# Kernel optimization log

Measured on AMD Instinct MI355X. Metric: run time of the kernel, lower is better.

Reference implementation:

```python
import jax, jax.numpy as jnp
import numpy as np

N, E, B = 50000, 800000, 64      # nodes, edges, graphs per branch
F_IN, C = 128, 128               # input feats, convolution_neurons
H = 2                            # hidden_layers
EPS = 1e-3                       # keras BatchNormalization epsilon


def _gconv(x, src, dst, W, b, gamma, beta):
    # Spektral GeneralConv: linear -> gather(src) -> scatter-sum(dst) -> BN(inference, mean=0,var=1) -> relu
    h = x @ W + b                                            # [N, C]
    agg = jax.ops.segment_sum(h[src], dst, num_segments=x.shape[0])  # [N, C]
    agg = agg * (gamma / np.float32(np.sqrt(1.0 + EPS))) + beta
    return jax.nn.relu(agg)


def _avg_pool(x, seg):
    s = jax.ops.segment_sum(x, seg, num_segments=B)          # [B, C]
    cnt = jax.ops.segment_sum(jnp.ones((x.shape[0],), x.dtype), seg, num_segments=B)
    return s / jnp.maximum(cnt, 1.0)[:, None]


def setup_inputs() -> dict:
    key = jax.random.key(0)
    ks = jax.random.split(key, 12)

    def glorot(k, shp):
        lim = float(np.sqrt(6.0 / (shp[0] + shp[1])))
        return jax.random.uniform(k, shp, jnp.float32, -lim, lim)

    inp = {}
    inp["x1"] = jax.random.normal(ks[0], (N, F_IN), jnp.float32)
    inp["x2"] = jax.random.normal(ks[1], (N, F_IN), jnp.float32)
    inp["edges1"] = jax.random.randint(ks[2], (2, E), 0, N)
    inp["edges2"] = jax.random.randint(ks[3], (2, E), 0, N)
    inp["seg1"] = jnp.sort(jax.random.randint(ks[4], (N,), 0, B))
    inp["seg2"] = jnp.sort(jax.random.randint(ks[5], (N,), 0, B))
    # branch 1: GeneralConv(128) then GeneralConv(64)
    inp["W1a"], inp["b1a"] = glorot(ks[6], (F_IN, C)), jnp.zeros((C,), jnp.float32)
    inp["g1a"], inp["be1a"] = jnp.ones((C,), jnp.float32), jnp.zeros((C,), jnp.float32)
    inp["W1b"], inp["b1b"] = glorot(ks[7], (C, C // 2)), jnp.zeros((C // 2,), jnp.float32)
    inp["g1b"], inp["be1b"] = jnp.ones((C // 2,), jnp.float32), jnp.zeros((C // 2,), jnp.float32)
    # branch 2
    inp["W2a"], inp["b2a"] = glorot(ks[8], (F_IN, C)), jnp.zeros((C,), jnp.float32)
    inp["g2a"], inp["be2a"] = jnp.ones((C,), jnp.float32), jnp.zeros((C,), jnp.float32)
    inp["W2b"], inp["b2b"] = glorot(ks[9], (C, C // 2)), jnp.zeros((C // 2,), jnp.float32)
    inp["g2b"], inp["be2b"] = jnp.ones((C // 2,), jnp.float32), jnp.zeros((C // 2,), jnp.float32)
    # shared hidden dense + output head
    inp["Wd"], inp["bd"] = glorot(ks[10], (C, C)), jnp.zeros((C,), jnp.float32)
    inp["Wo"], inp["bo"] = glorot(ks[11], (C, 1)), jnp.zeros((1,), jnp.float32)
    return inp


def reference(x1, x2, edges1, edges2, seg1, seg2,
              W1a, b1a, g1a, be1a, W1b, b1b, g1b, be1b,
              W2a, b2a, g2a, be2a, W2b, b2b, g2b, be2b,
              Wd, bd, Wo, bo):
    h1 = _gconv(x1, edges1[0], edges1[1], W1a, b1a, g1a, be1a)   # [N, 128]
    h1 = _gconv(h1, edges1[0], edges1[1], W1b, b1b, g1b, be1b)   # [N, 64]
    p1 = _avg_pool(h1, seg1)                                      # [B, 64]
    h2 = _gconv(x2, edges2[0], edges2[1], W2a, b2a, g2a, be2a)
    h2 = _gconv(h2, edges2[0], edges2[1], W2b, b2b, g2b, be2b)
    p2 = _avg_pool(h2, seg2)
    out = jnp.concatenate([p1, p2], axis=-1)                      # [B, 128]
    for _ in range(H):  # shared Dense(128, relu) applied hidden_layers times
        out = jax.nn.relu(out @ Wd + bd)
    return jax.nn.sigmoid(out @ Wo + bo)                          # [B, 1]
```

## Files before the change

kernel.cpp:

```cpp
#include <hip/hip_runtime.h>
#include <math.h>

#define GS    512
#define GSH   9
#define NGMAX 128
#define FCAP  48
#define SCAP  10240


__global__ __launch_bounds__(1024) void bin_kernel(
    const int* __restrict__ s1, const int* __restrict__ d1,
    const int* __restrict__ s2, const int* __restrict__ d2,
    int* __restrict__ gcur, int* __restrict__ pairs, int E, int G1) {
  __shared__ int fifo[NGMAX][FCAP];
  __shared__ int fcnt[NGMAX];
  __shared__ int fbase[NGMAX];
  __shared__ int fpre[NGMAX + 1];
  const int* src = blockIdx.y ? s2 : s1;
  const int* dst = blockIdx.y ? d2 : d1;
  int gboff = blockIdx.y * G1;
  int tid = threadIdx.x;
  if (tid < NGMAX) fcnt[tid] = 0;
  __syncthreads();
  int e0 = blockIdx.x * 4096;
  for (int r = 0; r < 4; ++r) {
    int e = e0 + r * 1024 + tid;
    if (e < E) {
      int s = src[e], d = dst[e];
      int g = d >> GSH;
      int pk = s | ((d & (GS - 1)) << 17);
      int pos = atomicAdd(&fcnt[g], 1);
      if (pos < FCAP) fifo[g][pos] = pk;
      else {
        int gp = atomicAdd(&gcur[gboff + g], 1);
        pairs[(size_t)(gboff + g) * SCAP + gp] = pk;
      }
    }
    __syncthreads();
    if (tid < G1) {
      int c = fcnt[tid];
      if (c > FCAP) c = FCAP;
      fcnt[tid] = c;
      fbase[tid] = (c > 0) ? atomicAdd(&gcur[gboff + tid], c) : 0;
    }
    __syncthreads();
    if (tid == 0) {
      int acc = 0;
      for (int i = 0; i < G1; ++i) { fpre[i] = acc; acc += fcnt[i]; }
      fpre[G1] = acc;
    }
    __syncthreads();
    int T = fpre[G1];
    for (int t = tid; t < T; t += 1024) {
      int lo = 0, hi = G1;
      while (hi - lo > 1) { int mid = (lo + hi) >> 1; if (fpre[mid] <= t) lo = mid; else hi = mid; }
      int idx = t - fpre[lo];
      pairs[(size_t)(gboff + lo) * SCAP + fbase[lo] + idx] = fifo[lo][idx];
    }
    __syncthreads();
    if (tid < NGMAX) fcnt[tid] = 0;
    __syncthreads();
  }
}


__global__ __launch_bounds__(1024) void refine_kernel(
    const int* __restrict__ gcur, int* __restrict__ pairs,
    int* __restrict__ offs, int* __restrict__ counts, int N, int G1) {
  __shared__ int stg[SCAP];
  __shared__ int hist[GS];
  __shared__ int excl[GS];
  __shared__ int wtot[8];
  int gl = blockIdx.x, br = blockIdx.y;
  int g = br * G1 + gl;
  size_t rbase = (size_t)g * SCAP;
  int rcnt = gcur[g];
  if (rcnt > SCAP) rcnt = SCAP;
  int tid = threadIdx.x;
  if (tid < GS) hist[tid] = 0;
  __syncthreads();
  for (int i = tid; i < rcnt; i += 1024) {
    int pk = pairs[rbase + i];
    stg[i] = pk;
    atomicAdd(&hist[pk >> 17], 1);
  }
  __syncthreads();
  if (tid < GS) {
    int lane = tid & 63, wv = tid >> 6;
    int v = hist[tid];
    int inc = v;
    #pragma unroll
    for (int off = 1; off < 64; off <<= 1) {
      int t = __shfl_up(inc, off);
      if (lane >= off) inc += t;
    }
    excl[tid] = inc - v;
    if (lane == 63) wtot[wv] = inc;
  }
  __syncthreads();
  if (tid == 0) {
    int a = 0;
    #pragma unroll
    for (int w = 0; w < 8; ++w) { int t = wtot[w]; wtot[w] = a; a += t; }
  }
  __syncthreads();
  if (tid < GS) excl[tid] += wtot[tid >> 6];
  __syncthreads();
  int node0 = gl * GS;
  int nloc = N - node0; if (nloc > GS) nloc = GS;
  for (int j = tid; j < nloc; j += 1024) {
    offs[br * N + node0 + j] = (int)rbase + excl[j];
    counts[br * N + node0 + j] = hist[j];
  }
  __syncthreads();
  for (int i = tid; i < rcnt; i += 1024) {
    int pk = stg[i];
    int pos = atomicAdd(&excl[pk >> 17], 1);
    pairs[rbase + pos] = pk & 0x1FFFF;
  }
}


template <int COUT>
__global__ __launch_bounds__(256, 2) void gemm2_kernel(
    const float* __restrict__ X0, const float* __restrict__ X1,
    const float* __restrict__ W0, const float* __restrict__ W1,
    const float* __restrict__ bias0, const float* __restrict__ bias1,
    float* __restrict__ Y0, float* __restrict__ Y1, int nrows) {
  constexpr int CG = COUT / 4;
  constexpr int RG = 256 / CG;
  constexpr int BM = 64;
  constexpr int RPT = BM / RG;
  const float* X = blockIdx.y ? X1 : X0;
  const float* W = blockIdx.y ? W1 : W0;
  const float* bias = blockIdx.y ? bias1 : bias0;
  float* Y = blockIdx.y ? Y1 : Y0;
  __shared__ float xs[BM][132];
  int tid = threadIdx.x;
  int block_row = blockIdx.x * BM;
  for (int i = tid; i < BM * 32; i += 256) {
    int r = i >> 5, c4 = i & 31;
    int gr = block_row + r;
    float4 v = make_float4(0.f, 0.f, 0.f, 0.f);
    if (gr < nrows) v = reinterpret_cast<const float4*>(X + (size_t)gr * 128)[c4];
    *reinterpret_cast<float4*>(&xs[r][c4 * 4]) = v;
  }
  __syncthreads();
  int c0 = (tid % CG) * 4;
  int r0 = (tid / CG) * RPT;
  float acc[RPT][4] = {};
  #pragma unroll 2
  for (int k = 0; k < 128; k += 4) {
    float4 w0 = *reinterpret_cast<const float4*>(&W[(k + 0) * COUT + c0]);
    float4 w1 = *reinterpret_cast<const float4*>(&W[(k + 1) * COUT + c0]);
    float4 w2 = *reinterpret_cast<const float4*>(&W[(k + 2) * COUT + c0]);
    float4 w3 = *reinterpret_cast<const float4*>(&W[(k + 3) * COUT + c0]);
    #pragma unroll
    for (int i = 0; i < RPT; ++i) {
      float4 x = *reinterpret_cast<const float4*>(&xs[r0 + i][k]);
      acc[i][0] = fmaf(x.x, w0.x, acc[i][0]);
      acc[i][1] = fmaf(x.x, w0.y, acc[i][1]);
      acc[i][2] = fmaf(x.x, w0.z, acc[i][2]);
      acc[i][3] = fmaf(x.x, w0.w, acc[i][3]);
      acc[i][0] = fmaf(x.y, w1.x, acc[i][0]);
      acc[i][1] = fmaf(x.y, w1.y, acc[i][1]);
      acc[i][2] = fmaf(x.y, w1.z, acc[i][2]);
      acc[i][3] = fmaf(x.y, w1.w, acc[i][3]);
      acc[i][0] = fmaf(x.z, w2.x, acc[i][0]);
      acc[i][1] = fmaf(x.z, w2.y, acc[i][1]);
      acc[i][2] = fmaf(x.z, w2.z, acc[i][2]);
      acc[i][3] = fmaf(x.z, w2.w, acc[i][3]);
      acc[i][0] = fmaf(x.w, w3.x, acc[i][0]);
      acc[i][1] = fmaf(x.w, w3.y, acc[i][1]);
      acc[i][2] = fmaf(x.w, w3.z, acc[i][2]);
      acc[i][3] = fmaf(x.w, w3.w, acc[i][3]);
    }
  }
  float4 bv = *reinterpret_cast<const float4*>(&bias[c0]);
  #pragma unroll
  for (int i = 0; i < RPT; ++i) {
    int gr = block_row + r0 + i;
    if (gr < nrows) {
      float4 o;
      o.x = acc[i][0] + bv.x; o.y = acc[i][1] + bv.y;
      o.z = acc[i][2] + bv.z; o.w = acc[i][3] + bv.w;
      *reinterpret_cast<float4*>(&Y[(size_t)gr * COUT + c0]) = o;
    }
  }
}


__global__ __launch_bounds__(256) void agg128_kernel(
    const float* __restrict__ h, const int* __restrict__ offs,
    const int* __restrict__ counts, const int* __restrict__ csr_src,
    const float* __restrict__ gamma, const float* __restrict__ beta,
    float* __restrict__ out, int n) {
  int node = blockIdx.x * 4 + (threadIdx.x >> 6);
  if (node >= n) return;
  node = __builtin_amdgcn_readfirstlane(node);
  int ch = blockIdx.y;
  int lane = threadIdx.x & 63;
  int half = lane >> 5;
  int l5 = lane & 31;
  const float* hh = h + ch * 64;
  int beg = offs[node], cnt = counts[node];
  const int* lp = csr_src + beg;
  float a0 = 0.f, a1 = 0.f;
  for (int base = 0; base < cnt; base += 64) {
    int rem = cnt - base;
    int m = rem < 64 ? rem : 64;
    int idx = lp[base + (lane < m ? lane : m - 1)];
    int mfull = m & ~15;
    int j = 0;
    for (; j < mfull; j += 16) {
      float2 v[8];
      #pragma unroll
      for (int u = 0; u < 8; ++u) {
        int s = __shfl(idx, j + 2 * u + half);
        v[u] = *reinterpret_cast<const float2*>(hh + (size_t)s * 128 + l5 * 2);
      }
      #pragma unroll
      for (int u = 0; u < 8; ++u) { a0 += v[u].x; a1 += v[u].y; }
    }
    if (j < m) {
      float2 v[8];
      #pragma unroll
      for (int u = 0; u < 8; ++u) {
        int ed = j + 2 * u + half;
        int s = __shfl(idx, ed < m ? ed : m - 1);
        v[u] = *reinterpret_cast<const float2*>(hh + (size_t)s * 128 + l5 * 2);
      }
      #pragma unroll
      for (int u = 0; u < 8; ++u) {
        bool ok = (j + 2 * u + half) < m;
        a0 += ok ? v[u].x : 0.f;
        a1 += ok ? v[u].y : 0.f;
      }
    }
  }
  a0 += __shfl_xor(a0, 32);
  a1 += __shfl_xor(a1, 32);
  const float inv = 1.0f / sqrtf(1.0f + 1.0e-3f);
  if (half == 0) {
    float2 g = reinterpret_cast<const float2*>(gamma + ch * 64)[l5];
    float2 b = reinterpret_cast<const float2*>(beta + ch * 64)[l5];
    float2 o;
    o.x = fmaxf(fmaf(a0, g.x * inv, b.x), 0.f);
    o.y = fmaxf(fmaf(a1, g.y * inv, b.y), 0.f);
    *reinterpret_cast<float2*>(out + (size_t)node * 128 + ch * 64 + l5 * 2) = o;
  }
}


__global__ __launch_bounds__(256) void agg64_kernel(
    const float* __restrict__ h, const int* __restrict__ offs,
    const int* __restrict__ counts, const int* __restrict__ csr_src,
    const float* __restrict__ gamma, const float* __restrict__ beta,
    float* __restrict__ out, int n) {
  int node = blockIdx.x * 4 + (threadIdx.x >> 6);
  if (node >= n) return;
  node = __builtin_amdgcn_readfirstlane(node);
  int lane = threadIdx.x & 63;
  int half = lane >> 5;
  int l5 = lane & 31;
  int beg = offs[node], cnt = counts[node];
  const int* lp = csr_src + beg;
  float a0 = 0.f, a1 = 0.f;
  for (int base = 0; base < cnt; base += 64) {
    int rem = cnt - base;
    int m = rem < 64 ? rem : 64;
    int idx = lp[base + (lane < m ? lane : m - 1)];
    int mfull = m & ~15;
    int j = 0;
    for (; j < mfull; j += 16) {
      float2 v[8];
      #pragma unroll
      for (int u = 0; u < 8; ++u) {
        int s = __shfl(idx, j + 2 * u + half);
        v[u] = *reinterpret_cast<const float2*>(h + (size_t)s * 64 + l5 * 2);
      }
      #pragma unroll
      for (int u = 0; u < 8; ++u) { a0 += v[u].x; a1 += v[u].y; }
    }
    if (j < m) {
      float2 v[8];
      #pragma unroll
      for (int u = 0; u < 8; ++u) {
        int ed = j + 2 * u + half;
        int s = __shfl(idx, ed < m ? ed : m - 1);
        v[u] = *reinterpret_cast<const float2*>(h + (size_t)s * 64 + l5 * 2);
      }
      #pragma unroll
      for (int u = 0; u < 8; ++u) {
        bool ok = (j + 2 * u + half) < m;
        a0 += ok ? v[u].x : 0.f;
        a1 += ok ? v[u].y : 0.f;
      }
    }
  }
  a0 += __shfl_xor(a0, 32);
  a1 += __shfl_xor(a1, 32);
  const float inv = 1.0f / sqrtf(1.0f + 1.0e-3f);
  if (half == 0) {
    float2 g = reinterpret_cast<const float2*>(gamma)[l5];
    float2 b = reinterpret_cast<const float2*>(beta)[l5];
    float2 o;
    o.x = fmaxf(fmaf(a0, g.x * inv, b.x), 0.f);
    o.y = fmaxf(fmaf(a1, g.y * inv, b.y), 0.f);
    *reinterpret_cast<float2*>(out + (size_t)node * 64 + l5 * 2) = o;
  }
}


__global__ __launch_bounds__(1024) void pool2_kernel(
    const float* __restrict__ h0, const float* __restrict__ h1,
    const int* __restrict__ seg0, const int* __restrict__ seg1,
    float* __restrict__ p, int n) {
  const float* h = blockIdx.y ? h1 : h0;
  const int* seg = blockIdx.y ? seg1 : seg0;
  float* pb = p + blockIdx.y * 64 * 64;
  int g = blockIdx.x;
  int lo, hi;
  { int l = 0, r = n; while (l < r) { int m = (l + r) >> 1; if (seg[m] < g) l = m + 1; else r = m; } lo = l; }
  { int l = 0, r = n; while (l < r) { int m = (l + r) >> 1; if (seg[m] < g + 1) l = m + 1; else r = m; } hi = l; }
  int c = threadIdx.x & 63;
  int sub = threadIdx.x >> 6;
  float acc = 0.f;
  for (int i = lo + sub; i < hi; i += 16) acc += h[(size_t)i * 64 + c];
  __shared__ float red[16][64];
  red[sub][c] = acc;
  __syncthreads();
  if (sub == 0) {
    float s = 0.f;
    #pragma unroll
    for (int k = 0; k < 16; ++k) s += red[k][c];
    float cnt = (float)(hi - lo);
    pb[g * 64 + c] = s / fmaxf(cnt, 1.0f);
  }
}


__global__ __launch_bounds__(512) void head_kernel(const float* __restrict__ p,
                                                   const float* __restrict__ Wd,
                                                   const float* __restrict__ bd,
                                                   const float* __restrict__ Wo,
                                                   const float* __restrict__ bo,
                                                   float* __restrict__ out) {
  __shared__ float cur[64][128];
  __shared__ float nxt[64][128];
  int tid = threadIdx.x;
  const float* p1 = p;
  const float* p2 = p + 64 * 64;
  for (int i = tid; i < 64 * 128; i += 512) {
    int r = i >> 7, c = i & 127;
    cur[r][c] = (c < 64) ? p1[r * 64 + c] : p2[r * 64 + (c - 64)];
  }
  __syncthreads();
  int c0 = (tid & 31) * 4;
  int r0 = (tid >> 5) * 4;
  for (int layer = 0; layer < 2; ++layer) {
    float acc[4][4] = {};
    #pragma unroll 4
    for (int k = 0; k < 128; ++k) {
      float4 w = *reinterpret_cast<const float4*>(&Wd[k * 128 + c0]);
      #pragma unroll
      for (int i = 0; i < 4; ++i) {
        float x = cur[r0 + i][k];
        acc[i][0] = fmaf(x, w.x, acc[i][0]);
        acc[i][1] = fmaf(x, w.y, acc[i][1]);
        acc[i][2] = fmaf(x, w.z, acc[i][2]);
        acc[i][3] = fmaf(x, w.w, acc[i][3]);
      }
    }
    float4 bv = *reinterpret_cast<const float4*>(&bd[c0]);
    __syncthreads();
    #pragma unroll
    for (int i = 0; i < 4; ++i) {
      float4 o;
      o.x = fmaxf(acc[i][0] + bv.x, 0.f);
      o.y = fmaxf(acc[i][1] + bv.y, 0.f);
      o.z = fmaxf(acc[i][2] + bv.z, 0.f);
      o.w = fmaxf(acc[i][3] + bv.w, 0.f);
      *reinterpret_cast<float4*>(&nxt[r0 + i][c0]) = o;
    }
    __syncthreads();
    for (int i = tid; i < 64 * 128; i += 512) (&cur[0][0])[i] = (&nxt[0][0])[i];
    __syncthreads();
  }
  int wv = tid >> 6, lane = tid & 63;
  for (int r = wv; r < 64; r += 8) {
    float v = cur[r][lane] * Wo[lane] + cur[r][64 + lane] * Wo[64 + lane];
    #pragma unroll
    for (int off = 32; off; off >>= 1) v += __shfl_down(v, off);
    if (lane == 0) out[r] = 1.0f / (1.0f + expf(-(v + bo[0])));
  }
}


extern "C" void kernel_launch(void* const* d_in, const int* in_sizes, int n_in,
                              void* d_out, int out_size, void* d_ws, size_t ws_size,
                              hipStream_t stream) {
  const float* x1  = (const float*)d_in[0];
  const float* x2  = (const float*)d_in[1];
  const int* e1    = (const int*)d_in[2];
  const int* e2    = (const int*)d_in[3];
  const int* seg1  = (const int*)d_in[4];
  const int* seg2  = (const int*)d_in[5];
  const float* W1a = (const float*)d_in[6];  const float* b1a = (const float*)d_in[7];
  const float* g1a = (const float*)d_in[8];  const float* be1a = (const float*)d_in[9];
  const float* W1b = (const float*)d_in[10]; const float* b1b = (const float*)d_in[11];
  const float* g1b = (const float*)d_in[12]; const float* be1b = (const float*)d_in[13];
  const float* W2a = (const float*)d_in[14]; const float* b2a = (const float*)d_in[15];
  const float* g2a = (const float*)d_in[16]; const float* be2a = (const float*)d_in[17];
  const float* W2b = (const float*)d_in[18]; const float* b2b = (const float*)d_in[19];
  const float* g2b = (const float*)d_in[20]; const float* be2b = (const float*)d_in[21];
  const float* Wd  = (const float*)d_in[22]; const float* bd  = (const float*)d_in[23];
  const float* Wo  = (const float*)d_in[24]; const float* bo  = (const float*)d_in[25];
  float* out = (float*)d_out;

  const int N = in_sizes[0] / 128;
  const int E = in_sizes[2] / 2;
  const int G1 = (N + GS - 1) >> GSH;
  const int G  = 2 * G1;

  char* ws = (char*)d_ws;
  size_t off = 0;
  auto alloc = [&](size_t bytes) -> void* {
    void* ptr = ws + off;
    off += (bytes + 255) & ~(size_t)255;
    return ptr;
  };
  float* h0   = (float*)alloc((size_t)N * 128 * sizeof(float));
  float* h1   = (float*)alloc((size_t)N * 128 * sizeof(float));
  float* ag0  = (float*)alloc((size_t)N * 128 * sizeof(float));
  float* ag1  = (float*)alloc((size_t)N * 128 * sizeof(float));
  int* pairs  = (int*)alloc((size_t)G * SCAP * sizeof(int));
  int* offs   = (int*)alloc((size_t)(2 * N) * sizeof(int));
  int* counts = (int*)alloc((size_t)(2 * N) * sizeof(int));
  int* gcur   = (int*)alloc((size_t)(G + 8) * sizeof(int));
  float* pbuf = (float*)alloc(2 * 64 * 64 * sizeof(float));
  (void)ws_size; (void)n_in; (void)out_size;

  hipMemsetAsync(gcur, 0, (size_t)(G + 8) * sizeof(int), stream);
  {
    dim3 gb((E + 4095) / 4096, 2);
    bin_kernel<<<gb, 1024, 0, stream>>>(e1, e1 + E, e2, e2 + E, gcur, pairs, E, G1);
    dim3 gr(G1, 2);
    refine_kernel<<<gr, 1024, 0, stream>>>(gcur, pairs, offs, counts, N, G1);
  }

  const int* offs0 = offs;       const int* cnts0 = counts;
  const int* offs1 = offs + N;   const int* cnts1 = counts + N;

  {
    dim3 gg((N + 63) / 64, 2);
    gemm2_kernel<128><<<gg, 256, 0, stream>>>(x1, x2, W1a, W2a, b1a, b2a, h0, h1, N);
  }
  {
    dim3 ga((N + 3) / 4, 2);
    agg128_kernel<<<ga, 256, 0, stream>>>(h0, offs0, cnts0, pairs, g1a, be1a, ag0, N);
    agg128_kernel<<<ga, 256, 0, stream>>>(h1, offs1, cnts1, pairs, g2a, be2a, ag1, N);
  }
  {
    dim3 gg((N + 63) / 64, 2);
    gemm2_kernel<64><<<gg, 256, 0, stream>>>(ag0, ag1, W1b, W2b, b1b, b2b, h0, h1, N);
  }
  agg64_kernel<<<(N + 3) / 4, 256, 0, stream>>>(h0, offs0, cnts0, pairs, g1b, be1b, ag0, N);
  agg64_kernel<<<(N + 3) / 4, 256, 0, stream>>>(h1, offs1, cnts1, pairs, g2b, be2b, ag1, N);
  {
    dim3 gp(64, 2);
    pool2_kernel<<<gp, 1024, 0, stream>>>(ag0, ag1, seg1, seg2, pbuf, N);
  }
  head_kernel<<<1, 512, 0, stream>>>(pbuf, Wd, bd, Wo, bo, out);
}
```

Before: 336.6 us.

## Slice aggregation by 16-column chunks with 16 nodes per wavefront

```diff
diff --git a/kernel.cpp b/kernel.cpp
--- a/kernel.cpp
+++ b/kernel.cpp
@@ -135,7 +135,7 @@
   const float* W = blockIdx.y ? W1 : W0;
   const float* bias = blockIdx.y ? bias1 : bias0;
   float* Y = blockIdx.y ? Y1 : Y0;
-  __shared__ float xs[BM][132];
+  __shared__ float xs[BM][128];
   int tid = threadIdx.x;
   int block_row = blockIdx.x * BM;
   for (int i = tid; i < BM * 32; i += 256) {
@@ -190,124 +190,56 @@
 }
 
 
-__global__ __launch_bounds__(256) void agg128_kernel(
+template <int C, int NSL>
+__global__ __launch_bounds__(1024) void agg_sl_kernel(
     const float* __restrict__ h, const int* __restrict__ offs,
-    const int* __restrict__ counts, const int* __restrict__ csr_src,
+    const int* __restrict__ counts, const int* __restrict__ csr,
     const float* __restrict__ gamma, const float* __restrict__ beta,
     float* __restrict__ out, int n) {
-  int node = blockIdx.x * 4 + (threadIdx.x >> 6);
-  if (node >= n) return;
-  node = __builtin_amdgcn_readfirstlane(node);
-  int ch = blockIdx.y;
-  int lane = threadIdx.x & 63;
-  int half = lane >> 5;
-  int l5 = lane & 31;
-  const float* hh = h + ch * 64;
-  int beg = offs[node], cnt = counts[node];
-  const int* lp = csr_src + beg;
-  float a0 = 0.f, a1 = 0.f;
-  for (int base = 0; base < cnt; base += 64) {
-    int rem = cnt - base;
-    int m = rem < 64 ? rem : 64;
-    int idx = lp[base + (lane < m ? lane : m - 1)];
-    int mfull = m & ~15;
-    int j = 0;
-    for (; j < mfull; j += 16) {
-      float2 v[8];
-      #pragma unroll
-      for (int u = 0; u < 8; ++u) {
-        int s = __shfl(idx, j + 2 * u + half);
-        v[u] = *reinterpret_cast<const float2*>(hh + (size_t)s * 128 + l5 * 2);
-      }
-      #pragma unroll
-      for (int u = 0; u < 8; ++u) { a0 += v[u].x; a1 += v[u].y; }
-    }
-    if (j < m) {
-      float2 v[8];
-      #pragma unroll
-      for (int u = 0; u < 8; ++u) {
-        int ed = j + 2 * u + half;
-        int s = __shfl(idx, ed < m ? ed : m - 1);
-        v[u] = *reinterpret_cast<const float2*>(hh + (size_t)s * 128 + l5 * 2);
-      }
-      #pragma unroll
-      for (int u = 0; u < 8; ++u) {
-        bool ok = (j + 2 * u + half) < m;
-        a0 += ok ? v[u].x : 0.f;
-        a1 += ok ? v[u].y : 0.f;
-      }
-    }
-  }
-  a0 += __shfl_xor(a0, 32);
-  a1 += __shfl_xor(a1, 32);
-  const float inv = 1.0f / sqrtf(1.0f + 1.0e-3f);
-  if (half == 0) {
-    float2 g = reinterpret_cast<const float2*>(gamma + ch * 64)[l5];
-    float2 b = reinterpret_cast<const float2*>(beta + ch * 64)[l5];
-    float2 o;
-    o.x = fmaxf(fmaf(a0, g.x * inv, b.x), 0.f);
-    o.y = fmaxf(fmaf(a1, g.y * inv, b.y), 0.f);
-    *reinterpret_cast<float2*>(out + (size_t)node * 128 + ch * 64 + l5 * 2) = o;
-  }
-}
-
-
-__global__ __launch_bounds__(256) void agg64_kernel(
-    const float* __restrict__ h, const int* __restrict__ offs,
-    const int* __restrict__ counts, const int* __restrict__ csr_src,
-    const float* __restrict__ gamma, const float* __restrict__ beta,
-    float* __restrict__ out, int n) {
-  int node = blockIdx.x * 4 + (threadIdx.x >> 6);
-  if (node >= n) return;
-  node = __builtin_amdgcn_readfirstlane(node);
-  int lane = threadIdx.x & 63;
-  int half = lane >> 5;
-  int l5 = lane & 31;
-  int beg = offs[node], cnt = counts[node];
-  const int* lp = csr_src + beg;
-  float a0 = 0.f, a1 = 0.f;
-  for (int base = 0; base < cnt; base += 64) {
-    int rem = cnt - base;
-    int m = rem < 64 ? rem : 64;
-    int idx = lp[base + (lane < m ? lane : m - 1)];
-    int mfull = m & ~15;
-    int j = 0;
-    for (; j < mfull; j += 16) {
-      float2 v[8];
-      #pragma unroll
-      for (int u = 0; u < 8; ++u) {
-        int s = __shfl(idx, j + 2 * u + half);
-        v[u] = *reinterpret_cast<const float2*>(h + (size_t)s * 64 + l5 * 2);
-      }
-      #pragma unroll
-      for (int u = 0; u < 8; ++u) { a0 += v[u].x; a1 += v[u].y; }
-    }
-    if (j < m) {
-      float2 v[8];
-      #pragma unroll
-      for (int u = 0; u < 8; ++u) {
-        int ed = j + 2 * u + half;
-        int s = __shfl(idx, ed < m ? ed : m - 1);
-        v[u] = *reinterpret_cast<const float2*>(h + (size_t)s * 64 + l5 * 2);
-      }
-      #pragma unroll
-      for (int u = 0; u < 8; ++u) {
-        bool ok = (j + 2 * u + half) < m;
-        a0 += ok ? v[u].x : 0.f;
-        a1 += ok ? v[u].y : 0.f;
-      }
-    }
-  }
-  a0 += __shfl_xor(a0, 32);
-  a1 += __shfl_xor(a1, 32);
-  const float inv = 1.0f / sqrtf(1.0f + 1.0e-3f);
-  if (half == 0) {
-    float2 g = reinterpret_cast<const float2*>(gamma)[l5];
-    float2 b = reinterpret_cast<const float2*>(beta)[l5];
-    float2 o;
-    o.x = fmaxf(fmaf(a0, g.x * inv, b.x), 0.f);
-    o.y = fmaxf(fmaf(a1, g.y * inv, b.y), 0.f);
-    *reinterpret_cast<float2*>(out + (size_t)node * 64 + l5 * 2) = o;
+  int slice = blockIdx.x & (NSL - 1);
+  int nodeblk = blockIdx.x / NSL;
+  int tid = threadIdx.x;
+  int wv = tid >> 6, lane = tid & 63;
+  int grp = lane >> 2, c4 = lane & 3;
+  int node = nodeblk * 256 + wv * 16 + grp;
+  bool live = node < n;
+  int nd = live ? node : n - 1;
+  int beg = offs[nd];
+  int cnt = live ? counts[nd] : 0;
+  int elast = cnt > 0 ? cnt - 1 : 0;
+  int mx = cnt;
+  #pragma unroll
+  for (int off = 4; off < 64; off <<= 1) {
+    int t = __shfl_xor(mx, off);
+    mx = t > mx ? t : mx;
+  }
+  const float* hp = h + slice * 16 + c4 * 4;
+  float4 a = make_float4(0.f, 0.f, 0.f, 0.f);
+  for (int eb = 0; eb < mx; eb += 4) {
+    int ee = eb + c4;
+    ee = ee < elast ? ee : elast;
+    int idx = csr[beg + ee];
+    #pragma unroll
+    for (int u = 0; u < 4; ++u) {
+      int s = __shfl(idx, grp * 4 + u);
+      float4 v = *reinterpret_cast<const float4*>(hp + (size_t)s * C);
+      bool ok = (eb + u) < cnt;
+      a.x += ok ? v.x : 0.f;
+      a.y += ok ? v.y : 0.f;
+      a.z += ok ? v.z : 0.f;
+      a.w += ok ? v.w : 0.f;
+    }
+  }
+  if (live) {
+    const float inv = 1.0f / sqrtf(1.0f + 1.0e-3f);
+    float4 gv = *reinterpret_cast<const float4*>(gamma + slice * 16 + c4 * 4);
+    float4 bv = *reinterpret_cast<const float4*>(beta + slice * 16 + c4 * 4);
+    float4 o;
+    o.x = fmaxf(fmaf(a.x, gv.x * inv, bv.x), 0.f);
+    o.y = fmaxf(fmaf(a.y, gv.y * inv, bv.y), 0.f);
+    o.z = fmaxf(fmaf(a.z, gv.z * inv, bv.z), 0.f);
+    o.w = fmaxf(fmaf(a.w, gv.w * inv, bv.w), 0.f);
+    *reinterpret_cast<float4*>(out + (size_t)node * C + slice * 16 + c4 * 4) = o;
   }
 }
 
@@ -422,6 +354,7 @@
   const int E = in_sizes[2] / 2;
   const int G1 = (N + GS - 1) >> GSH;
   const int G  = 2 * G1;
+  const int NB = (N + 255) / 256;
 
   char* ws = (char*)d_ws;
   size_t off = 0;
@@ -449,24 +382,18 @@
     refine_kernel<<<gr, 1024, 0, stream>>>(gcur, pairs, offs, counts, N, G1);
   }
 
-  const int* offs0 = offs;       const int* cnts0 = counts;
-  const int* offs1 = offs + N;   const int* cnts1 = counts + N;
-
   {
     dim3 gg((N + 63) / 64, 2);
     gemm2_kernel<128><<<gg, 256, 0, stream>>>(x1, x2, W1a, W2a, b1a, b2a, h0, h1, N);
   }
-  {
-    dim3 ga((N + 3) / 4, 2);
-    agg128_kernel<<<ga, 256, 0, stream>>>(h0, offs0, cnts0, pairs, g1a, be1a, ag0, N);
-    agg128_kernel<<<ga, 256, 0, stream>>>(h1, offs1, cnts1, pairs, g2a, be2a, ag1, N);
-  }
+  agg_sl_kernel<128, 8><<<NB * 8, 1024, 0, stream>>>(h0, offs, counts, pairs, g1a, be1a, ag0, N);
+  agg_sl_kernel<128, 8><<<NB * 8, 1024, 0, stream>>>(h1, offs + N, counts + N, pairs, g2a, be2a, ag1, N);
   {
     dim3 gg((N + 63) / 64, 2);
     gemm2_kernel<64><<<gg, 256, 0, stream>>>(ag0, ag1, W1b, W2b, b1b, b2b, h0, h1, N);
   }
-  agg64_kernel<<<(N + 3) / 4, 256, 0, stream>>>(h0, offs0, cnts0, pairs, g1b, be1b, ag0, N);
-  agg64_kernel<<<(N + 3) / 4, 256, 0, stream>>>(h1, offs1, cnts1, pairs, g2b, be2b, ag1, N);
+  agg_sl_kernel<64, 4><<<NB * 4, 1024, 0, stream>>>(h0, offs, counts, pairs, g1b, be1b, ag0, N);
+  agg_sl_kernel<64, 4><<<NB * 4, 1024, 0, stream>>>(h1, offs + N, counts + N, pairs, g2b, be2b, ag1, N);
   {
     dim3 gp(64, 2);
     pool2_kernel<<<gp, 1024, 0, stream>>>(ag0, ag1, seg1, seg2, pbuf, N);
```

New measurement: 439.2 us. +30.5%, slower.

## Overlap next-branch GEMM with current aggregation in fused mixed-role kernels

Applied to the files above, without the earlier changes.

```diff
diff --git a/kernel.cpp b/kernel.cpp
--- a/kernel.cpp
+++ b/kernel.cpp
@@ -121,193 +121,133 @@
 }
 
 
-template <int COUT>
-__global__ __launch_bounds__(256, 2) void gemm2_kernel(
-    const float* __restrict__ X0, const float* __restrict__ X1,
-    const float* __restrict__ W0, const float* __restrict__ W1,
-    const float* __restrict__ bias0, const float* __restrict__ bias1,
-    float* __restrict__ Y0, float* __restrict__ Y1, int nrows) {
-  constexpr int CG = COUT / 4;
-  constexpr int RG = 256 / CG;
-  constexpr int BM = 64;
-  constexpr int RPT = BM / RG;
-  const float* X = blockIdx.y ? X1 : X0;
-  const float* W = blockIdx.y ? W1 : W0;
-  const float* bias = blockIdx.y ? bias1 : bias0;
-  float* Y = blockIdx.y ? Y1 : Y0;
-  __shared__ float xs[BM][132];
+template <int CA, int COUT>
+__global__ __launch_bounds__(256, 2) void mix_kernel(
+    const float* __restrict__ hA, const int* __restrict__ offsA,
+    const int* __restrict__ cntsA, const int* __restrict__ csr,
+    const float* __restrict__ gamA, const float* __restrict__ betA,
+    float* __restrict__ outA,
+    const float* __restrict__ XB, const float* __restrict__ WB,
+    const float* __restrict__ biasB, float* __restrict__ YB,
+    int n, int nGemm, int nTot) {
+  __shared__ float xs[64][128];
+  long long b = blockIdx.x;
+  int gBefore = (int)((b * nGemm) / nTot);
+  int gAfter = (int)(((b + 1) * nGemm) / nTot);
   int tid = threadIdx.x;
-  int block_row = blockIdx.x * BM;
-  for (int i = tid; i < BM * 32; i += 256) {
-    int r = i >> 5, c4 = i & 31;
-    int gr = block_row + r;
-    float4 v = make_float4(0.f, 0.f, 0.f, 0.f);
-    if (gr < nrows) v = reinterpret_cast<const float4*>(X + (size_t)gr * 128)[c4];
-    *reinterpret_cast<float4*>(&xs[r][c4 * 4]) = v;
-  }
-  __syncthreads();
-  int c0 = (tid % CG) * 4;
-  int r0 = (tid / CG) * RPT;
-  float acc[RPT][4] = {};
-  #pragma unroll 2
-  for (int k = 0; k < 128; k += 4) {
-    float4 w0 = *reinterpret_cast<const float4*>(&W[(k + 0) * COUT + c0]);
-    float4 w1 = *reinterpret_cast<const float4*>(&W[(k + 1) * COUT + c0]);
-    float4 w2 = *reinterpret_cast<const float4*>(&W[(k + 2) * COUT + c0]);
-    float4 w3 = *reinterpret_cast<const float4*>(&W[(k + 3) * COUT + c0]);
+  if (gAfter > gBefore) {
+    constexpr int CG = COUT / 4;
+    constexpr int RG = 256 / CG;
+    constexpr int BM = 64;
+    constexpr int RPT = BM / RG;
+    int block_row = gBefore * BM;
+    for (int i = tid; i < BM * 32; i += 256) {
+      int r = i >> 5, c4 = i & 31;
+      int gr = block_row + r;
+      float4 v = make_float4(0.f, 0.f, 0.f, 0.f);
+      if (gr < n) v = reinterpret_cast<const float4*>(XB + (size_t)gr * 128)[c4];
+      *reinterpret_cast<float4*>(&xs[r][c4 * 4]) = v;
+    }
+    __syncthreads();
+    int c0 = (tid % CG) * 4;
+    int r0 = (tid / CG) * RPT;
+    float acc[RPT][4] = {};
+    #pragma unroll 2
+    for (int k = 0; k < 128; k += 4) {
+      float4 w0 = *reinterpret_cast<const float4*>(&WB[(k + 0) * COUT + c0]);
+      float4 w1 = *reinterpret_cast<const float4*>(&WB[(k + 1) * COUT + c0]);
+      float4 w2 = *reinterpret_cast<const float4*>(&WB[(k + 2) * COUT + c0]);
+      float4 w3 = *reinterpret_cast<const float4*>(&WB[(k + 3) * COUT + c0]);
+      #pragma unroll
+      for (int i = 0; i < RPT; ++i) {
+        float4 x = *reinterpret_cast<const float4*>(&xs[r0 + i][k]);
+        acc[i][0] = fmaf(x.x, w0.x, acc[i][0]);
+        acc[i][1] = fmaf(x.x, w0.y, acc[i][1]);
+        acc[i][2] = fmaf(x.x, w0.z, acc[i][2]);
+        acc[i][3] = fmaf(x.x, w0.w, acc[i][3]);
+        acc[i][0] = fmaf(x.y, w1.x, acc[i][0]);
+        acc[i][1] = fmaf(x.y, w1.y, acc[i][1]);
+        acc[i][2] = fmaf(x.y, w1.z, acc[i][2]);
+        acc[i][3] = fmaf(x.y, w1.w, acc[i][3]);
+        acc[i][0] = fmaf(x.z, w2.x, acc[i][0]);
+        acc[i][1] = fmaf(x.z, w2.y, acc[i][1]);
+        acc[i][2] = fmaf(x.z, w2.z, acc[i][2]);
+        acc[i][3] = fmaf(x.z, w2.w, acc[i][3]);
+        acc[i][0] = fmaf(x.w, w3.x, acc[i][0]);
+        acc[i][1] = fmaf(x.w, w3.y, acc[i][1]);
+        acc[i][2] = fmaf(x.w, w3.z, acc[i][2]);
+        acc[i][3] = fmaf(x.w, w3.w, acc[i][3]);
+      }
+    }
+    float4 bv = *reinterpret_cast<const float4*>(&biasB[c0]);
     #pragma unroll
     for (int i = 0; i < RPT; ++i) {
-      float4 x = *reinterpret_cast<const float4*>(&xs[r0 + i][k]);
-      acc[i][0] = fmaf(x.x, w0.x, acc[i][0]);
-      acc[i][1] = fmaf(x.x, w0.y, acc[i][1]);
-      acc[i][2] = fmaf(x.x, w0.z, acc[i][2]);
-      acc[i][3] = fmaf(x.x, w0.w, acc[i][3]);
-      acc[i][0] = fmaf(x.y, w1.x, acc[i][0]);
-      acc[i][1] = fmaf(x.y, w1.y, acc[i][1]);
-      acc[i][2] = fmaf(x.y, w1.z, acc[i][2]);
-      acc[i][3] = fmaf(x.y, w1.w, acc[i][3]);
-      acc[i][0] = fmaf(x.z, w2.x, acc[i][0]);
-      acc[i][1] = fmaf(x.z, w2.y, acc[i][1]);
-      acc[i][2] = fmaf(x.z, w2.z, acc[i][2]);
-      acc[i][3] = fmaf(x.z, w2.w, acc[i][3]);
-      acc[i][0] = fmaf(x.w, w3.x, acc[i][0]);
-      acc[i][1] = fmaf(x.w, w3.y, acc[i][1]);
-      acc[i][2] = fmaf(x.w, w3.z, acc[i][2]);
-      acc[i][3] = fmaf(x.w, w3.w, acc[i][3]);
-    }
-  }
-  float4 bv = *reinterpret_cast<const float4*>(&bias[c0]);
-  #pragma unroll
-  for (int i = 0; i < RPT; ++i) {
-    int gr = block_row + r0 + i;
-    if (gr < nrows) {
-      float4 o;
-      o.x = acc[i][0] + bv.x; o.y = acc[i][1] + bv.y;
-      o.z = acc[i][2] + bv.z; o.w = acc[i][3] + bv.w;
-      *reinterpret_cast<float4*>(&Y[(size_t)gr * COUT + c0]) = o;
-    }
-  }
-}
-
-
-__global__ __launch_bounds__(256) void agg128_kernel(
-    const float* __restrict__ h, const int* __restrict__ offs,
-    const int* __restrict__ counts, const int* __restrict__ csr_src,
-    const float* __restrict__ gamma, const float* __restrict__ beta,
-    float* __restrict__ out, int n) {
-  int node = blockIdx.x * 4 + (threadIdx.x >> 6);
-  if (node >= n) return;
-  node = __builtin_amdgcn_readfirstlane(node);
-  int ch = blockIdx.y;
-  int lane = threadIdx.x & 63;
-  int half = lane >> 5;
-  int l5 = lane & 31;
-  const float* hh = h + ch * 64;
-  int beg = offs[node], cnt = counts[node];
-  const int* lp = csr_src + beg;
-  float a0 = 0.f, a1 = 0.f;
-  for (int base = 0; base < cnt; base += 64) {
-    int rem = cnt - base;
-    int m = rem < 64 ? rem : 64;
-    int idx = lp[base + (lane < m ? lane : m - 1)];
-    int mfull = m & ~15;
-    int j = 0;
-    for (; j < mfull; j += 16) {
-      float2 v[8];
-      #pragma unroll
-      for (int u = 0; u < 8; ++u) {
-        int s = __shfl(idx, j + 2 * u + half);
-        v[u] = *reinterpret_cast<const float2*>(hh + (size_t)s * 128 + l5 * 2);
-      }
-      #pragma unroll
-      for (int u = 0; u < 8; ++u) { a0 += v[u].x; a1 += v[u].y; }
-    }
-    if (j < m) {
-      float2 v[8];
-      #pragma unroll
-      for (int u = 0; u < 8; ++u) {
-        int ed = j + 2 * u + half;
-        int s = __shfl(idx, ed < m ? ed : m - 1);
-        v[u] = *reinterpret_cast<const float2*>(hh + (size_t)s * 128 + l5 * 2);
-      }
-      #pragma unroll
-      for (int u = 0; u < 8; ++u) {
-        bool ok = (j + 2 * u + half) < m;
-        a0 += ok ? v[u].x : 0.f;
-        a1 += ok ? v[u].y : 0.f;
-      }
-    }
-  }
-  a0 += __shfl_xor(a0, 32);
-  a1 += __shfl_xor(a1, 32);
-  const float inv = 1.0f / sqrtf(1.0f + 1.0e-3f);
-  if (half == 0) {
-    float2 g = reinterpret_cast<const float2*>(gamma + ch * 64)[l5];
-    float2 b = reinterpret_cast<const float2*>(beta + ch * 64)[l5];
-    float2 o;
-    o.x = fmaxf(fmaf(a0, g.x * inv, b.x), 0.f);
-    o.y = fmaxf(fmaf(a1, g.y * inv, b.y), 0.f);
-    *reinterpret_cast<float2*>(out + (size_t)node * 128 + ch * 64 + l5 * 2) = o;
-  }
-}
-
-
-__global__ __launch_bounds__(256) void agg64_kernel(
-    const float* __restrict__ h, const int* __restrict__ offs,
-    const int* __restrict__ counts, const int* __restrict__ csr_src,
-    const float* __restrict__ gamma, const float* __restrict__ beta,
-    float* __restrict__ out, int n) {
-  int node = blockIdx.x * 4 + (threadIdx.x >> 6);
-  if (node >= n) return;
-  node = __builtin_amdgcn_readfirstlane(node);
-  int lane = threadIdx.x & 63;
-  int half = lane >> 5;
-  int l5 = lane & 31;
-  int beg = offs[node], cnt = counts[node];
-  const int* lp = csr_src + beg;
-  float a0 = 0.f, a1 = 0.f;
-  for (int base = 0; base < cnt; base += 64) {
-    int rem = cnt - base;
-    int m = rem < 64 ? rem : 64;
-    int idx = lp[base + (lane < m ? lane : m - 1)];
-    int mfull = m & ~15;
-    int j = 0;
-    for (; j < mfull; j += 16) {
-      float2 v[8];
-      #pragma unroll
-      for (int u = 0; u < 8; ++u) {
-        int s = __shfl(idx, j + 2 * u + half);
-        v[u] = *reinterpret_cast<const float2*>(h + (size_t)s * 64 + l5 * 2);
-      }
-      #pragma unroll
-      for (int u = 0; u < 8; ++u) { a0 += v[u].x; a1 += v[u].y; }
-    }
-    if (j < m) {
-      float2 v[8];
-      #pragma unroll
-      for (int u = 0; u < 8; ++u) {
-        int ed = j + 2 * u + half;
-        int s = __shfl(idx, ed < m ? ed : m - 1);
-        v[u] = *reinterpret_cast<const float2*>(h + (size_t)s * 64 + l5 * 2);
-      }
-      #pragma unroll
-      for (int u = 0; u < 8; ++u) {
-        bool ok = (j + 2 * u + half) < m;
-        a0 += ok ? v[u].x : 0.f;
-        a1 += ok ? v[u].y : 0.f;
-      }
-    }
-  }
-  a0 += __shfl_xor(a0, 32);
-  a1 += __shfl_xor(a1, 32);
-  const float inv = 1.0f / sqrtf(1.0f + 1.0e-3f);
-  if (half == 0) {
-    float2 g = reinterpret_cast<const float2*>(gamma)[l5];
-    float2 b = reinterpret_cast<const float2*>(beta)[l5];
-    float2 o;
-    o.x = fmaxf(fmaf(a0, g.x * inv, b.x), 0.f);
-    o.y = fmaxf(fmaf(a1, g.y * inv, b.y), 0.f);
-    *reinterpret_cast<float2*>(out + (size_t)node * 64 + l5 * 2) = o;
+      int gr = block_row + r0 + i;
+      if (gr < n) {
+        float4 o;
+        o.x = acc[i][0] + bv.x; o.y = acc[i][1] + bv.y;
+        o.z = acc[i][2] + bv.z; o.w = acc[i][3] + bv.w;
+        *reinterpret_cast<float4*>(&YB[(size_t)gr * COUT + c0]) = o;
+      }
+    }
+  } else {
+    int aid = (int)b - gBefore;
+    int nb4 = (n + 3) >> 2;
+    int ch = aid / nb4;
+    int nblk = aid - ch * nb4;
+    int node = nblk * 4 + (tid >> 6);
+    if (node >= n) return;
+    node = __builtin_amdgcn_readfirstlane(node);
+    int lane = tid & 63;
+    int half = lane >> 5;
+    int l5 = lane & 31;
+    const float* hh = hA + ch * 64;
+    int beg = offsA[node], cnt = cntsA[node];
+    const int* lp = csr + beg;
+    float a0 = 0.f, a1 = 0.f;
+    for (int base = 0; base < cnt; base += 64) {
+      int rem = cnt - base;
+      int m = rem < 64 ? rem : 64;
+      int idx = lp[base + (lane < m ? lane : m - 1)];
+      int mfull = m & ~15;
+      int j = 0;
+      for (; j < mfull; j += 16) {
+        float2 v[8];
+        #pragma unroll
+        for (int u = 0; u < 8; ++u) {
+          int s = __shfl(idx, j + 2 * u + half);
+          v[u] = *reinterpret_cast<const float2*>(hh + (size_t)s * CA + l5 * 2);
+        }
+        #pragma unroll
+        for (int u = 0; u < 8; ++u) { a0 += v[u].x; a1 += v[u].y; }
+      }
+      if (j < m) {
+        float2 v[8];
+        #pragma unroll
+        for (int u = 0; u < 8; ++u) {
+          int ed = j + 2 * u + half;
+          int s = __shfl(idx, ed < m ? ed : m - 1);
+          v[u] = *reinterpret_cast<const float2*>(hh + (size_t)s * CA + l5 * 2);
+        }
+        #pragma unroll
+        for (int u = 0; u < 8; ++u) {
+          bool ok = (j + 2 * u + half) < m;
+          a0 += ok ? v[u].x : 0.f;
+          a1 += ok ? v[u].y : 0.f;
+        }
+      }
+    }
+    a0 += __shfl_xor(a0, 32);
+    a1 += __shfl_xor(a1, 32);
+    const float inv = 1.0f / sqrtf(1.0f + 1.0e-3f);
+    if (half == 0) {
+      float2 g = reinterpret_cast<const float2*>(gamA + ch * 64)[l5];
+      float2 be = reinterpret_cast<const float2*>(betA + ch * 64)[l5];
+      float2 o;
+      o.x = fmaxf(fmaf(a0, g.x * inv, be.x), 0.f);
+      o.y = fmaxf(fmaf(a1, g.y * inv, be.y), 0.f);
+      *reinterpret_cast<float2*>(outA + (size_t)node * CA + ch * 64 + l5 * 2) = o;
+    }
   }
 }
 
@@ -422,6 +362,8 @@
   const int E = in_sizes[2] / 2;
   const int G1 = (N + GS - 1) >> GSH;
   const int G  = 2 * G1;
+  const int nb4 = (N + 3) / 4;
+  const int GB  = (N + 63) / 64;
 
   char* ws = (char*)d_ws;
   size_t off = 0;
@@ -449,24 +391,31 @@
     refine_kernel<<<gr, 1024, 0, stream>>>(gcur, pairs, offs, counts, N, G1);
   }
 
-  const int* offs0 = offs;       const int* cnts0 = counts;
-  const int* offs1 = offs + N;   const int* cnts1 = counts + N;
-
+  mix_kernel<128, 128><<<GB, 256, 0, stream>>>(
+      h0, offs, counts, pairs, g1a, be1a, ag0,
+      x1, W1a, b1a, h0, N, GB, GB);
   {
-    dim3 gg((N + 63) / 64, 2);
-    gemm2_kernel<128><<<gg, 256, 0, stream>>>(x1, x2, W1a, W2a, b1a, b2a, h0, h1, N);
+    int nTot = nb4 * 2 + GB;
+    mix_kernel<128, 128><<<nTot, 256, 0, stream>>>(
+        h0, offs, counts, pairs, g1a, be1a, ag0,
+        x2, W2a, b2a, h1, N, GB, nTot);
   }
   {
-    dim3 ga((N + 3) / 4, 2);
-    agg128_kernel<<<ga, 256, 0, stream>>>(h0, offs0, cnts0, pairs, g1a, be1a, ag0, N);
-    agg128_kernel<<<ga, 256, 0, stream>>>(h1, offs1, cnts1, pairs, g2a, be2a, ag1, N);
+    int nTot = nb4 * 2 + GB;
+    mix_kernel<128, 64><<<nTot, 256, 0, stream>>>(
+        h1, offs + N, counts + N, pairs, g2a, be2a, ag1,
+        ag0, W1b, b1b, h0, N, GB, nTot);
   }
   {
-    dim3 gg((N + 63) / 64, 2);
-    gemm2_kernel<64><<<gg, 256, 0, stream>>>(ag0, ag1, W1b, W2b, b1b, b2b, h0, h1, N);
-  }
-  agg64_kernel<<<(N + 3) / 4, 256, 0, stream>>>(h0, offs0, cnts0, pairs, g1b, be1b, ag0, N);
-  agg64_kernel<<<(N + 3) / 4, 256, 0, stream>>>(h1, offs1, cnts1, pairs, g2b, be2b, ag1, N);
+    int nTot = nb4 + GB;
+    mix_kernel<64, 64><<<nTot, 256, 0, stream>>>(
+        h0, offs, counts, pairs, g1b, be1b, ag0,
+        ag1, W2b, b2b, h1, N, GB, nTot);
+  }
+  mix_kernel<64, 64><<<nb4, 256, 0, stream>>>(
+      h1, offs + N, counts + N, pairs, g2b, be2b, ag1,
+      x1, W1a, b1a, h0, N, 0, nb4);
+
   {
     dim3 gp(64, 2);
     pool2_kernel<<<gp, 1024, 0, stream>>>(ag0, ag1, seg1, seg2, pbuf, N);
```

Measured after the change: 426.0 us. 1.27x slower.
